# Optimization experiments

Hardware: AMD Instinct MI355X
Metric: run time of the kernel (lower is better)

The kernel has to match this reference:

```python
import jax, jax.numpy as jnp
import numpy as np

D_MODEL = 128; D_STATE = 64; D_CONV = 4; EXPAND = 2; HEADDIM = 32; NGROUPS = 1
D_INNER = EXPAND * D_MODEL            # 256
NHEADS = D_INNER // HEADDIM           # 8
CONV_DIM = D_INNER + 2 * NGROUPS * D_STATE   # 384 (x, B, C streams)
D_IN_PROJ = 2 * D_INNER + 2 * NGROUPS * D_STATE + NHEADS  # 648 (z, xBC, dt)
EPS = 1e-5


def setup_inputs() -> dict:
    key = jax.random.key(0)
    ks = jax.random.split(key, 8)
    B, L = 8, 4096
    x = jax.random.normal(ks[0], (B, L, D_MODEL), jnp.float32)
    norm_w = jnp.ones((D_MODEL,), jnp.float32)
    in_proj_w = jax.random.normal(ks[1], (D_IN_PROJ, D_MODEL), jnp.float32) * (D_MODEL ** -0.5)
    conv_w = jax.random.normal(ks[2], (CONV_DIM, D_CONV), jnp.float32) * (D_CONV ** -0.5)
    conv_b = jnp.zeros((CONV_DIM,), jnp.float32)
    dt_bias = jax.random.uniform(ks[3], (NHEADS,), jnp.float32, -4.0, -1.0)
    A_log = jnp.log(jax.random.uniform(ks[4], (NHEADS,), jnp.float32, 1.0, 16.0))
    D = jnp.ones((NHEADS,), jnp.float32)
    gnorm_w = jnp.ones((D_INNER,), jnp.float32)
    out_proj_w = jax.random.normal(ks[5], (D_MODEL, D_INNER), jnp.float32) * (D_INNER ** -0.5)
    return dict(x=x, norm_w=norm_w, in_proj_w=in_proj_w, conv_w=conv_w, conv_b=conv_b,
                dt_bias=dt_bias, A_log=A_log, D=D, gnorm_w=gnorm_w, out_proj_w=out_proj_w)


def _rmsnorm(x, w):
    return x * jax.lax.rsqrt(jnp.mean(x * x, axis=-1, keepdims=True) + EPS) * w


def _causal_dw_conv(x, w, b):
    # x: [B,L,C]; w: [C,K]; depthwise causal conv along L
    K = w.shape[1]
    xp = jnp.pad(x, ((0, 0), (K - 1, 0), (0, 0)))
    kern = jnp.transpose(w)[:, None, :]  # [K,1,C] for WIO with groups=C
    out = jax.lax.conv_general_dilated(
        xp, kern, window_strides=(1,), padding='VALID',
        dimension_numbers=('NWC', 'WIO', 'NWC'),
        feature_group_count=w.shape[0])
    return out + b


def _ssm(xh, dt, Bm, Cm, A):
    # xh: [B,L,H,P]; dt: [B,L,H]; Bm, Cm: [B,L,N]; A: [H]
    def step(h, inp):
        x_t, dt_t, B_t, C_t = inp
        dA = jnp.exp(dt_t * A)                                   # [B,H]
        h = h * dA[..., None, None] + (dt_t[..., None] * x_t)[..., None] * B_t[:, None, None, :]
        y = jnp.einsum('bhpn,bn->bhp', h, C_t)
        return h, y
    Bsz, L, H, P = xh.shape
    N = Bm.shape[-1]
    h0 = jnp.zeros((Bsz, H, P, N), xh.dtype)
    xs = (xh.transpose(1, 0, 2, 3), dt.transpose(1, 0, 2),
          Bm.transpose(1, 0, 2), Cm.transpose(1, 0, 2))
    _, ys = jax.lax.scan(step, h0, xs)
    return ys.transpose(1, 0, 2, 3)  # [B,L,H,P]


def reference(x, norm_w, in_proj_w, conv_w, conv_b, dt_bias, A_log, D, gnorm_w, out_proj_w):
    xn = _rmsnorm(x, norm_w)
    zxbcdt = xn @ in_proj_w.T                                    # [B,L,648]
    z, xBC, dt = jnp.split(zxbcdt, [D_INNER, D_INNER + CONV_DIM], axis=-1)
    dt = jax.nn.softplus(dt + dt_bias)                           # [B,L,H]
    xBC = jax.nn.silu(_causal_dw_conv(xBC, conv_w, conv_b))
    xs, Bm, Cm = jnp.split(xBC, [D_INNER, D_INNER + NGROUPS * D_STATE], axis=-1)
    Bsz, L, _ = x.shape
    xh = xs.reshape(Bsz, L, NHEADS, HEADDIM)
    A = -jnp.exp(A_log)                                          # [H]
    y = _ssm(xh, dt, Bm, Cm, A) + D[None, None, :, None] * xh    # D skip per head
    y = y.reshape(Bsz, L, D_INNER)
    y = _rmsnorm(y * jax.nn.silu(z), gnorm_w)                    # gated RMSNorm
    out = y @ out_proj_w.T
    return x + out
```

## Files before the change

### kernel.cpp

```cpp
#include <hip/hip_runtime.h>

#define DM    128
#define DI    256
#define NH    8
#define HD    32
#define NS    64
#define CDIM  384
#define DPROJ 648
#define LSEQ  4096
#define NB    8
#define NTOK  32768
#define LC    64
#define NC    64
#define EPSF  1e-5f
#define LOG2E 1.4426950408889634f

typedef __bf16 bf16;
typedef bf16  bf16x8 __attribute__((ext_vector_type(8)));
typedef bf16  bf16x4 __attribute__((ext_vector_type(4)));
typedef short short8 __attribute__((ext_vector_type(8)));
typedef float f32x4  __attribute__((ext_vector_type(4)));

__device__ __forceinline__ unsigned short f2bfbits(float f) {
    unsigned int u = __float_as_uint(f);
    unsigned int r = u + 0x7FFFu + ((u >> 16) & 1u);
    return (unsigned short)(r >> 16);
}
__device__ __forceinline__ float bfbits2f(unsigned short u) {
    return __uint_as_float(((unsigned int)u) << 16);
}

__global__ __launch_bounds__(256) void k_prep(const float* __restrict__ w1,
                                              const float* __restrict__ w2,
                                              const float* __restrict__ gw,
                                              unsigned short* __restrict__ w1g,
                                              unsigned short* __restrict__ w2f) {
    int i = blockIdx.x * 256 + threadIdx.x;
    if (i < 640 * DM) {
        int f = i >> 9, r = i & 511;
        int lane = r >> 3, jj = r & 7;
        int ns = f >> 2, kk = f & 3;
        int n = ns * 16 + (lane & 15), k = kk * 32 + (lane >> 4) * 8 + jj;
        w1g[i] = f2bfbits(w1[(size_t)n * DM + k]);
    } else {
        int j = i - 640 * DM;
        if (j < DM * DI) {
            int f = j >> 9, r = j & 511;
            int lane = r >> 3, jj = r & 7;
            int kk = f >> 3, nt = f & 7;
            int fr = lane & 15, ko = lane >> 4;
            int n = nt * 16 + fr, k = kk * 32 + ko * 8 + jj;
            w2f[j] = f2bfbits(w2[(size_t)n * DI + k] * gw[k]);
        }
    }
}

__global__ __launch_bounds__(256) void k_rmsdt(const float* __restrict__ x,
                                               const float* __restrict__ w,
                                               const float* __restrict__ w1,
                                               const float* __restrict__ dtb,
                                               unsigned short* __restrict__ xnb,
                                               float* __restrict__ dtf) {
    __shared__ float Xs[4][132];
    __shared__ float Wd[8][132];
    const int t = threadIdx.x;
    {
        int row = t >> 5, col = (t & 31) * 4;
        *(float4*)&Wd[row][col] = *(const float4*)(w1 + (size_t)(640 + row) * DM + col);
    }
    const int wave = t >> 6, lane = t & 63;
    const size_t row = (size_t)blockIdx.x * 4 + wave;
    const float* xr = x + row * DM + lane * 2;
    float v0 = xr[0], v1 = xr[1];
    float ss = v0 * v0 + v1 * v1;
    #pragma unroll
    for (int o = 32; o; o >>= 1) ss += __shfl_xor(ss, o);
    float r = rsqrtf(ss * (1.0f / DM) + EPSF);
    float o0 = v0 * r * w[lane * 2], o1 = v1 * r * w[lane * 2 + 1];
    Xs[wave][lane * 2] = o0; Xs[wave][lane * 2 + 1] = o1;
    ushort2 ob; ob.x = f2bfbits(o0); ob.y = f2bfbits(o1);
    *(ushort2*)(xnb + row * DM + lane * 2) = ob;
    __syncthreads();
    const int h = lane >> 3, ks = lane & 7;
    float acc = 0.f;
    #pragma unroll
    for (int i = 0; i < 4; i++) {
        float4 xv = *(const float4*)&Xs[wave][ks * 16 + i * 4];
        float4 wv = *(const float4*)&Wd[h][ks * 16 + i * 4];
        acc = fmaf(xv.x, wv.x, acc);
        acc = fmaf(xv.y, wv.y, acc);
        acc = fmaf(xv.z, wv.z, acc);
        acc = fmaf(xv.w, wv.w, acc);
    }
    acc += __shfl_xor(acc, 1);
    acc += __shfl_xor(acc, 2);
    acc += __shfl_xor(acc, 4);
    if (ks == 0) {
        float v = acc + dtb[h];
        dtf[row * NH + h] = (v > 20.f) ? v : log1pf(expf(v));
    }
}

__global__ __launch_bounds__(256, 4) void k_gemm1(const unsigned short* __restrict__ A,
                                                  const unsigned short* __restrict__ w1g,
                                                  unsigned short* __restrict__ zb,
                                                  unsigned short* __restrict__ xbc) {
    const int t = threadIdx.x;
    const int m0 = blockIdx.x * 64;
    const int wave = t >> 6, lane = t & 63;
    const int wm = wave >> 1, wn = wave & 1;
    const int fr = lane & 15, ko = lane >> 4;
    bf16x8 a[2][4];
    #pragma unroll
    for (int mt = 0; mt < 2; mt++)
        #pragma unroll
        for (int kk = 0; kk < 4; kk++)
            a[mt][kk] = *(const bf16x8*)(A + (size_t)(m0 + wm * 32 + mt * 16 + fr) * DM
                                           + kk * 32 + ko * 8);
    for (int nt = 0; nt < 10; nt++) {
        const unsigned short* wb = w1g + (((size_t)(nt * 4 + wn * 2) * 4) << 9) + lane * 8;
        f32x4 acc[2][2] = {};
        #pragma unroll
        for (int kk = 0; kk < 4; kk++) {
            bf16x8 b0 = *(const bf16x8*)(wb + ((size_t)kk << 9));
            bf16x8 b1 = *(const bf16x8*)(wb + ((size_t)(4 + kk) << 9));
            acc[0][0] = __builtin_amdgcn_mfma_f32_16x16x32_bf16(a[0][kk], b0, acc[0][0], 0, 0, 0);
            acc[1][0] = __builtin_amdgcn_mfma_f32_16x16x32_bf16(a[1][kk], b0, acc[1][0], 0, 0, 0);
            acc[0][1] = __builtin_amdgcn_mfma_f32_16x16x32_bf16(a[0][kk], b1, acc[0][1], 0, 0, 0);
            acc[1][1] = __builtin_amdgcn_mfma_f32_16x16x32_bf16(a[1][kk], b1, acc[1][1], 0, 0, 0);
        }
        unsigned short* dst; int ld, nc0;
        if (nt < 4) { dst = zb;  ld = DI;   nc0 = nt * 64; }
        else        { dst = xbc; ld = CDIM; nc0 = nt * 64 - 256; }
        #pragma unroll
        for (int mt = 0; mt < 2; mt++)
            #pragma unroll
            for (int ntt = 0; ntt < 2; ntt++) {
                int n = nc0 + wn * 32 + ntt * 16 + fr;
                #pragma unroll
                for (int rr = 0; rr < 4; rr++) {
                    int m = m0 + wm * 32 + mt * 16 + ko * 4 + rr;
                    dst[(size_t)m * ld + n] = f2bfbits(acc[mt][ntt][rr]);
                }
            }
    }
}

__global__ __launch_bounds__(384) void k_conv(const unsigned short* __restrict__ xbc,
                                              const float* __restrict__ cw,
                                              const float* __restrict__ cb,
                                              unsigned short* __restrict__ bcA,
                                              unsigned short* __restrict__ xT,
                                              unsigned short* __restrict__ bT) {
    __shared__ __align__(16) unsigned short L[320][72];
    const int c = threadIdx.x;
    const int t0 = blockIdx.x * 64;
    const int l0 = t0 & (LSEQ - 1);
    float4 wv = *(const float4*)(cw + c * 4);
    float bias = cb[c];
    const unsigned short* in = xbc + (size_t)t0 * CDIM + c;
    float h1 = 0.f, h2 = 0.f, h3 = 0.f;
    if (l0) {
        h1 = bfbits2f(in[-CDIM]);
        h2 = bfbits2f(in[-2 * CDIM]);
        h3 = bfbits2f(in[-3 * CDIM]);
    }
    short8 pk;
    #pragma unroll 8
    for (int t = 0; t < 64; t++) {
        float x0 = bfbits2f(in[(size_t)t * CDIM]);
        float acc = bias;
        acc = fmaf(x0, wv.w, acc);
        acc = fmaf(h1, wv.z, acc);
        acc = fmaf(h2, wv.y, acc);
        acc = fmaf(h3, wv.x, acc);
        float s = acc / (1.f + expf(-acc));
        unsigned short us = f2bfbits(s);
        if (c >= 256) bcA[(size_t)(t0 + t) * 128 + (c - 256)] = us;
        pk[t & 7] = (short)us;
        if (c < 320 && (t & 7) == 7) *(short8*)&L[c][t - 7] = pk;
        h3 = h2; h2 = h1; h1 = x0;
    }
    __syncthreads();
    #pragma unroll
    for (int it = 0; it < 7; it++) {
        int idx = it * 384 + c;
        if (idx < 2560) {
            int row = idx >> 3, tc = (idx & 7) * 8;
            short8 v = *(const short8*)&L[row][tc];
            unsigned short* dst = (row < 256)
                ? xT + (size_t)row * NTOK + t0 + tc
                : bT + (size_t)(row - 256) * NTOK + t0 + tc;
            *(short8*)dst = v;
        }
    }
}

__global__ __launch_bounds__(256, 4) void k_ssd1(const unsigned short* __restrict__ bT,
                                                 const unsigned short* __restrict__ xT,
                                                 const float* __restrict__ dtf,
                                                 const float* __restrict__ alog,
                                                 unsigned short* __restrict__ hst,
                                                 float* __restrict__ dAp) {
    __shared__ __align__(16) float wl[4][64];
    const int bh = blockIdx.x >> 4, cg = blockIdx.x & 15;
    const int b = bh >> 3, h = bh & 7;
    const int wave = threadIdx.x >> 6, lane = threadIdx.x & 63;
    const int c = cg * 4 + wave;
    const size_t tok0 = (size_t)b * LSEQ + c * LC;
    const float A = -expf(alog[h]);
    float dt = dtf[(tok0 + lane) * NH + h];
    float q = dt * A * LOG2E;
    #pragma unroll
    for (int o = 1; o <= 32; o <<= 1) {
        float tmp = __shfl_up(q, o);
        if (lane >= o) q += tmp;
    }
    float qL = __shfl(q, 63);
    wl[wave][lane] = exp2f(qL - q) * dt;
    if (lane == 0) dAp[(size_t)bh * NC + c] = exp2f(qL);
    __syncthreads();
    const int m = lane & 15, ko = lane >> 4;
    f32x4 hacc[4][2] = {};
    #pragma unroll
    for (int kh = 0; kh < 2; kh++) {
        bf16x8 xb[2];
        #pragma unroll
        for (int pi = 0; pi < 2; pi++)
            xb[pi] = *(const bf16x8*)(xT + (size_t)(h * HD + pi * 16 + m) * NTOK + tok0 + kh * 32 + ko * 8);
        f32x4 w0 = *(const f32x4*)&wl[wave][kh * 32 + ko * 8];
        f32x4 w1 = *(const f32x4*)&wl[wave][kh * 32 + ko * 8 + 4];
        #pragma unroll
        for (int ni = 0; ni < 4; ni++) {
            bf16x8 bv = *(const bf16x8*)(bT + (size_t)(ni * 16 + m) * NTOK + tok0 + kh * 32 + ko * 8);
            bf16x8 af;
            #pragma unroll
            for (int j = 0; j < 4; j++) af[j] = (bf16)((float)bv[j] * w0[j]);
            #pragma unroll
            for (int j = 0; j < 4; j++) af[4 + j] = (bf16)((float)bv[4 + j] * w1[j]);
            #pragma unroll
            for (int pi = 0; pi < 2; pi++)
                hacc[ni][pi] = __builtin_amdgcn_mfma_f32_16x16x32_bf16(af, xb[pi], hacc[ni][pi], 0, 0, 0);
        }
    }
    unsigned short* hb = hst + (((size_t)bh * NC + c) << 11);
    #pragma unroll
    for (int ni = 0; ni < 4; ni++)
        #pragma unroll
        for (int pi = 0; pi < 2; pi++) {
            bf16x4 pv;
            #pragma unroll
            for (int r = 0; r < 4; r++) pv[r] = (bf16)hacc[ni][pi][r];
            *(bf16x4*)(hb + (pi * 16 + m) * 64 + ni * 16 + ko * 4) = pv;
        }
}

__global__ __launch_bounds__(256) void k_ssm2(unsigned short* __restrict__ hst,
                                              const float* __restrict__ dAp) {
    __shared__ float dl[NC];
    const int bh = blockIdx.x >> 3, seg = blockIdx.x & 7;
    const int s = seg * 256 + threadIdx.x;
    if (threadIdx.x < NC) dl[threadIdx.x] = dAp[(size_t)bh * NC + threadIdx.x];
    __syncthreads();
    unsigned short* p = hst + ((size_t)bh * NC << 11) + s;
    float r = 0.f;
    float v0 = bfbits2f(p[0]);
    float v1 = bfbits2f(p[(size_t)1 << 11]);
    float v2 = bfbits2f(p[(size_t)2 << 11]);
    float v3 = bfbits2f(p[(size_t)3 << 11]);
    for (int c = 0; c < NC; c += 4) {
        float t;
        t = v0; if (c + 4 < NC) v0 = bfbits2f(p[(size_t)(c + 4) << 11]);
        p[(size_t)c << 11] = f2bfbits(r);       r = fmaf(r, dl[c], t);
        t = v1; if (c + 5 < NC) v1 = bfbits2f(p[(size_t)(c + 5) << 11]);
        p[(size_t)(c + 1) << 11] = f2bfbits(r); r = fmaf(r, dl[c + 1], t);
        t = v2; if (c + 6 < NC) v2 = bfbits2f(p[(size_t)(c + 6) << 11]);
        p[(size_t)(c + 2) << 11] = f2bfbits(r); r = fmaf(r, dl[c + 2], t);
        t = v3; if (c + 7 < NC) v3 = bfbits2f(p[(size_t)(c + 7) << 11]);
        p[(size_t)(c + 3) << 11] = f2bfbits(r); r = fmaf(r, dl[c + 3], t);
    }
}

__global__ __launch_bounds__(256, 2) void k_ssd3(const unsigned short* __restrict__ bcA,
                                                 const unsigned short* __restrict__ xT,
                                                 const float* __restrict__ dtf,
                                                 const float* __restrict__ alog,
                                                 const unsigned short* __restrict__ hst,
                                                 const float* __restrict__ Dw,
                                                 unsigned short* __restrict__ ybb) {
    __shared__ __align__(16) bf16 Pl[4][64 * 72];
    __shared__ __align__(16) float ql[4][64];
    __shared__ __align__(16) float dl[4][64];
    const int bh = blockIdx.x >> 4, cg = blockIdx.x & 15;
    const int b = bh >> 3, h = bh & 7;
    const int wave = threadIdx.x >> 6, lane = threadIdx.x & 63;
    const int c = cg * 4 + wave;
    const size_t tok0 = (size_t)b * LSEQ + c * LC;
    const float A = -expf(alog[h]);
    const float Dh = Dw[h];
    float dt = dtf[(tok0 + lane) * NH + h];
    float q = dt * A * LOG2E;
    #pragma unroll
    for (int o = 1; o <= 32; o <<= 1) {
        float tmp = __shfl_up(q, o);
        if (lane >= o) q += tmp;
    }
    ql[wave][lane] = q;
    dl[wave][lane] = dt;
    const int m = lane & 15, ko = lane >> 4;
    bf16x8 cf[4][2];
    #pragma unroll
    for (int ti = 0; ti < 4; ti++)
        #pragma unroll
        for (int kh = 0; kh < 2; kh++)
            cf[ti][kh] = *(const bf16x8*)(bcA + (tok0 + ti * 16 + m) * 128 + 64 + kh * 32 + ko * 8);
    f32x4 gt[4][4] = {};
    #pragma unroll
    for (int kh = 0; kh < 2; kh++) {
        bf16x8 bfg[4];
        #pragma unroll
        for (int si = 0; si < 4; si++)
            bfg[si] = *(const bf16x8*)(bcA + (tok0 + si * 16 + m) * 128 + kh * 32 + ko * 8);
        #pragma unroll
        for (int ti = 0; ti < 4; ti++)
            #pragma unroll
            for (int si = 0; si < 4; si++)
                gt[ti][si] = __builtin_amdgcn_mfma_f32_16x16x32_bf16(bfg[si], cf[ti][kh], gt[ti][si], 0, 0, 0);
    }
    __syncthreads();
    float qt[4];
    #pragma unroll
    for (int ti = 0; ti < 4; ti++) qt[ti] = ql[wave][ti * 16 + m];
    #pragma unroll
    for (int si = 0; si < 4; si++) {
        f32x4 qs = *(const f32x4*)&ql[wave][si * 16 + ko * 4];
        f32x4 ds = *(const f32x4*)&dl[wave][si * 16 + ko * 4];
        #pragma unroll
        for (int ti = 0; ti < 4; ti++) {
            bf16x4 pv = {};
            if (si <= ti) {
                const int t = ti * 16 + m;
                #pragma unroll
                for (int r = 0; r < 4; r++) {
                    int s = si * 16 + ko * 4 + r;
                    float p = 0.f;
                    if (s <= t) {
                        p = exp2f(qt[ti] - qs[r]) * ds[r] * gt[ti][si][r];
                        if (s == t) p += Dh;
                    }
                    pv[r] = (bf16)p;
                }
            }
            *(bf16x4*)&Pl[wave][(ti * 16 + m) * 72 + si * 16 + ko * 4] = pv;
        }
    }
    __syncthreads();
    f32x4 et[4];
    #pragma unroll
    for (int ti = 0; ti < 4; ti++) {
        f32x4 qv = *(const f32x4*)&ql[wave][ti * 16 + ko * 4];
        #pragma unroll
        for (int r = 0; r < 4; r++) et[ti][r] = exp2f(qv[r]);
    }
    const size_t hbase = ((size_t)bh * NC + c) << 11;
    f32x4 ya[4][2] = {}, ua[4][2] = {};
    #pragma unroll
    for (int kh = 0; kh < 2; kh++) {
        bf16x8 xb[2], hb2[2];
        #pragma unroll
        for (int pi = 0; pi < 2; pi++) {
            xb[pi]  = *(const bf16x8*)(xT + (size_t)(h * HD + pi * 16 + m) * NTOK + tok0 + kh * 32 + ko * 8);
            hb2[pi] = *(const bf16x8*)(hst + hbase + (pi * 16 + m) * 64 + kh * 32 + ko * 8);
        }
        #pragma unroll
        for (int ti = 0; ti < 4; ti++) {
            bf16x8 pa = *(const bf16x8*)&Pl[wave][(ti * 16 + m) * 72 + kh * 32 + ko * 8];
            #pragma unroll
            for (int pi = 0; pi < 2; pi++) {
                ya[ti][pi] = __builtin_amdgcn_mfma_f32_16x16x32_bf16(pa, xb[pi], ya[ti][pi], 0, 0, 0);
                ua[ti][pi] = __builtin_amdgcn_mfma_f32_16x16x32_bf16(cf[ti][kh], hb2[pi], ua[ti][pi], 0, 0, 0);
            }
        }
    }
    unsigned short* yrow = ybb + tok0 * DI + h * HD;
    #pragma unroll
    for (int ti = 0; ti < 4; ti++)
        #pragma unroll
        for (int pi = 0; pi < 2; pi++)
            #pragma unroll
            for (int r = 0; r < 4; r++) {
                int t = ti * 16 + ko * 4 + r;
                yrow[(size_t)t * DI + pi * 16 + m] =
                    f2bfbits(ya[ti][pi][r] + et[ti][r] * ua[ti][pi][r]);
            }
}

__global__ __launch_bounds__(256, 4) void k_gemm2g(const unsigned short* __restrict__ ybb,
                                                   const unsigned short* __restrict__ zb,
                                                   const unsigned short* __restrict__ w2f,
                                                   const float* __restrict__ xin,
                                                   float* __restrict__ out) {
    const int t = threadIdx.x;
    const int wave = t >> 6, lane = t & 63;
    const int fr = lane & 15, ko = lane >> 4;
    const int m0 = blockIdx.x * 64 + wave * 16;
    const size_t rowo = (size_t)(m0 + fr) * DI;
    float ss = 0.f;
    bf16x8 gb[8];
    #pragma unroll
    for (int kk = 0; kk < 8; kk++) {
        int co = kk * 32 + ko * 8;
        bf16x8 yv = *(const bf16x8*)(ybb + rowo + co);
        bf16x8 zv = *(const bf16x8*)(zb + rowo + co);
        #pragma unroll
        for (int j = 0; j < 8; j++) {
            float z = (float)zv[j];
            float g = (float)yv[j] * (z / (1.f + expf(-z)));
            ss += g * g;
            gb[kk][j] = (bf16)g;
        }
    }
    ss += __shfl_xor(ss, 16);
    ss += __shfl_xor(ss, 32);
    const float rs = rsqrtf(ss * (1.0f / DI) + EPSF);
    #pragma unroll
    for (int kk = 0; kk < 8; kk++)
        #pragma unroll
        for (int j = 0; j < 8; j++)
            gb[kk][j] = (bf16)((float)gb[kk][j] * rs);
    const unsigned short* wp = w2f + (size_t)lane * 8;
    f32x4 acc[8] = {};
    #pragma unroll
    for (int kk = 0; kk < 8; kk++) {
        #pragma unroll
        for (int nt = 0; nt < 8; nt++) {
            bf16x8 bfr = *(const bf16x8*)(wp + (((size_t)kk * 8 + nt) << 9));
            acc[nt] = __builtin_amdgcn_mfma_f32_16x16x32_bf16(gb[kk], bfr, acc[nt], 0, 0, 0);
        }
    }
    #pragma unroll
    for (int nt = 0; nt < 8; nt++) {
        int n = nt * 16 + fr;
        #pragma unroll
        for (int rr = 0; rr < 4; rr++) {
            int m = m0 + ko * 4 + rr;
            out[(size_t)m * DM + n] = xin[(size_t)m * DM + n] + acc[nt][rr];
        }
    }
}

extern "C" void kernel_launch(void* const* d_in, const int* in_sizes, int n_in,
                              void* d_out, int out_size, void* d_ws, size_t ws_size,
                              hipStream_t stream) {
    const float* x   = (const float*)d_in[0];
    const float* nw  = (const float*)d_in[1];
    const float* w1  = (const float*)d_in[2];
    const float* cw  = (const float*)d_in[3];
    const float* cb  = (const float*)d_in[4];
    const float* dtb = (const float*)d_in[5];
    const float* al  = (const float*)d_in[6];
    const float* Dw  = (const float*)d_in[7];
    const float* gw  = (const float*)d_in[8];
    const float* w2  = (const float*)d_in[9];
    float* out = (float*)d_out;

    float* ws = (float*)d_ws;
    float*  dAp = ws;
    float*  dtf = dAp + NB * NH * NC;
    unsigned short* hst = (unsigned short*)(dtf + (size_t)NTOK * NH);
    unsigned short* zb  = hst + (size_t)NB * NH * NC * 2048;
    unsigned short* xbc = zb + (size_t)NTOK * DI;
    unsigned short* bcA = xbc + (size_t)NTOK * CDIM;
    unsigned short* xT  = bcA + (size_t)NTOK * 128;
    unsigned short* bT  = xT + (size_t)DI * NTOK;
    unsigned short* ybb = bT + (size_t)64 * NTOK;
    unsigned short* w1g = ybb + (size_t)NTOK * DI;
    unsigned short* w2f = w1g + (size_t)640 * DM;
    unsigned short* xnb = ybb;

    k_prep<<<(640 * DM + DM * DI + 255) / 256, 256, 0, stream>>>(w1, w2, gw, w1g, w2f);
    k_rmsdt<<<NTOK / 4, 256, 0, stream>>>(x, nw, w1, dtb, xnb, dtf);
    k_gemm1<<<NTOK / 64, 256, 0, stream>>>(xnb, w1g, zb, xbc);
    k_conv<<<NTOK / 64, 384, 0, stream>>>(xbc, cw, cb, bcA, xT, bT);
    k_ssd1<<<NB * NH * (NC / 4), 256, 0, stream>>>(bT, xT, dtf, al, hst, dAp);
    k_ssm2<<<NB * NH * 8, 256, 0, stream>>>(hst, dAp);
    k_ssd3<<<NB * NH * (NC / 4), 256, 0, stream>>>(bcA, xT, dtf, al, hst, Dw, ybb);
    k_gemm2g<<<NTOK / 64, 256, 0, stream>>>(ybb, zb, w2f, x, out);
}
```

Before: 197.1 us.

## Fuse RMSNorm and dt projection into GEMM1 and drop intra-wave barriers

```diff
diff --git a/kernel.cpp b/kernel.cpp
--- a/kernel.cpp
+++ b/kernel.cpp
@@ -55,68 +55,74 @@
     }
 }
 
-__global__ __launch_bounds__(256) void k_rmsdt(const float* __restrict__ x,
-                                               const float* __restrict__ w,
-                                               const float* __restrict__ w1,
-                                               const float* __restrict__ dtb,
-                                               unsigned short* __restrict__ xnb,
-                                               float* __restrict__ dtf) {
-    __shared__ float Xs[4][132];
+__global__ __launch_bounds__(256, 4) void k_gemm1(const float* __restrict__ x,
+                                                  const float* __restrict__ nw,
+                                                  const float* __restrict__ w1,
+                                                  const float* __restrict__ dtb,
+                                                  const unsigned short* __restrict__ w1g,
+                                                  unsigned short* __restrict__ zb,
+                                                  unsigned short* __restrict__ xbc,
+                                                  float* __restrict__ dtf) {
+    __shared__ float Xs[64][132];
     __shared__ float Wd[8][132];
     const int t = threadIdx.x;
+    const int wave = t >> 6, lane = t & 63;
+    const int m0 = blockIdx.x * 64;
     {
         int row = t >> 5, col = (t & 31) * 4;
         *(float4*)&Wd[row][col] = *(const float4*)(w1 + (size_t)(640 + row) * DM + col);
     }
-    const int wave = t >> 6, lane = t & 63;
-    const size_t row = (size_t)blockIdx.x * 4 + wave;
-    const float* xr = x + row * DM + lane * 2;
-    float v0 = xr[0], v1 = xr[1];
-    float ss = v0 * v0 + v1 * v1;
-    #pragma unroll
-    for (int o = 32; o; o >>= 1) ss += __shfl_xor(ss, o);
-    float r = rsqrtf(ss * (1.0f / DM) + EPSF);
-    float o0 = v0 * r * w[lane * 2], o1 = v1 * r * w[lane * 2 + 1];
-    Xs[wave][lane * 2] = o0; Xs[wave][lane * 2 + 1] = o1;
-    ushort2 ob; ob.x = f2bfbits(o0); ob.y = f2bfbits(o1);
-    *(ushort2*)(xnb + row * DM + lane * 2) = ob;
+    const float nw0 = nw[lane * 2], nw1 = nw[lane * 2 + 1];
+    #pragma unroll
+    for (int i = 0; i < 16; i++) {
+        int r = wave * 16 + i;
+        const float* xr = x + (size_t)(m0 + r) * DM + lane * 2;
+        float v0 = xr[0], v1 = xr[1];
+        float ss = v0 * v0 + v1 * v1;
+        #pragma unroll
+        for (int o = 32; o; o >>= 1) ss += __shfl_xor(ss, o);
+        float rs = rsqrtf(ss * (1.0f / DM) + EPSF);
+        Xs[r][lane * 2]     = v0 * rs * nw0;
+        Xs[r][lane * 2 + 1] = v1 * rs * nw1;
+    }
     __syncthreads();
-    const int h = lane >> 3, ks = lane & 7;
-    float acc = 0.f;
-    #pragma unroll
-    for (int i = 0; i < 4; i++) {
-        float4 xv = *(const float4*)&Xs[wave][ks * 16 + i * 4];
-        float4 wv = *(const float4*)&Wd[h][ks * 16 + i * 4];
-        acc = fmaf(xv.x, wv.x, acc);
-        acc = fmaf(xv.y, wv.y, acc);
-        acc = fmaf(xv.z, wv.z, acc);
-        acc = fmaf(xv.w, wv.w, acc);
-    }
-    acc += __shfl_xor(acc, 1);
-    acc += __shfl_xor(acc, 2);
-    acc += __shfl_xor(acc, 4);
-    if (ks == 0) {
-        float v = acc + dtb[h];
-        dtf[row * NH + h] = (v > 20.f) ? v : log1pf(expf(v));
-    }
-}
-
-__global__ __launch_bounds__(256, 4) void k_gemm1(const unsigned short* __restrict__ A,
-                                                  const unsigned short* __restrict__ w1g,
-                                                  unsigned short* __restrict__ zb,
-                                                  unsigned short* __restrict__ xbc) {
-    const int t = threadIdx.x;
-    const int m0 = blockIdx.x * 64;
-    const int wave = t >> 6, lane = t & 63;
+    {
+        const int h = lane >> 3, ks = lane & 7;
+        const float dtbh = dtb[h];
+        #pragma unroll
+        for (int i = 0; i < 16; i++) {
+            int r = wave * 16 + i;
+            float acc = 0.f;
+            #pragma unroll
+            for (int q = 0; q < 4; q++) {
+                float4 xv = *(const float4*)&Xs[r][ks * 16 + q * 4];
+                float4 wv = *(const float4*)&Wd[h][ks * 16 + q * 4];
+                acc = fmaf(xv.x, wv.x, acc); acc = fmaf(xv.y, wv.y, acc);
+                acc = fmaf(xv.z, wv.z, acc); acc = fmaf(xv.w, wv.w, acc);
+            }
+            acc += __shfl_xor(acc, 1);
+            acc += __shfl_xor(acc, 2);
+            acc += __shfl_xor(acc, 4);
+            if (ks == 0) {
+                float v = acc + dtbh;
+                dtf[(size_t)(m0 + r) * NH + h] = (v > 20.f) ? v : log1pf(expf(v));
+            }
+        }
+    }
     const int wm = wave >> 1, wn = wave & 1;
     const int fr = lane & 15, ko = lane >> 4;
     bf16x8 a[2][4];
     #pragma unroll
     for (int mt = 0; mt < 2; mt++)
         #pragma unroll
-        for (int kk = 0; kk < 4; kk++)
-            a[mt][kk] = *(const bf16x8*)(A + (size_t)(m0 + wm * 32 + mt * 16 + fr) * DM
-                                           + kk * 32 + ko * 8);
+        for (int kk = 0; kk < 4; kk++) {
+            const float* src = &Xs[wm * 32 + mt * 16 + fr][kk * 32 + ko * 8];
+            float4 lo = *(const float4*)src, hi = *(const float4*)(src + 4);
+            bf16x8 af;
+            af[0] = (bf16)lo.x; af[1] = (bf16)lo.y; af[2] = (bf16)lo.z; af[3] = (bf16)lo.w;
+            af[4] = (bf16)hi.x; af[5] = (bf16)hi.y; af[6] = (bf16)hi.z; af[7] = (bf16)hi.w;
+            a[mt][kk] = af;
+        }
     for (int nt = 0; nt < 10; nt++) {
         const unsigned short* wb = w1g + (((size_t)(nt * 4 + wn * 2) * 4) << 9) + lane * 8;
         f32x4 acc[2][2] = {};
@@ -219,7 +225,6 @@
     float qL = __shfl(q, 63);
     wl[wave][lane] = exp2f(qL - q) * dt;
     if (lane == 0) dAp[(size_t)bh * NC + c] = exp2f(qL);
-    __syncthreads();
     const int m = lane & 15, ko = lane >> 4;
     f32x4 hacc[4][2] = {};
     #pragma unroll
@@ -327,7 +332,6 @@
             for (int si = 0; si < 4; si++)
                 gt[ti][si] = __builtin_amdgcn_mfma_f32_16x16x32_bf16(bfg[si], cf[ti][kh], gt[ti][si], 0, 0, 0);
     }
-    __syncthreads();
     float qt[4];
     #pragma unroll
     for (int ti = 0; ti < 4; ti++) qt[ti] = ql[wave][ti * 16 + m];
@@ -354,7 +358,6 @@
             *(bf16x4*)&Pl[wave][(ti * 16 + m) * 72 + si * 16 + ko * 4] = pv;
         }
     }
-    __syncthreads();
     f32x4 et[4];
     #pragma unroll
     for (int ti = 0; ti < 4; ti++) {
@@ -476,11 +479,9 @@
     unsigned short* ybb = bT + (size_t)64 * NTOK;
     unsigned short* w1g = ybb + (size_t)NTOK * DI;
     unsigned short* w2f = w1g + (size_t)640 * DM;
-    unsigned short* xnb = ybb;
 
     k_prep<<<(640 * DM + DM * DI + 255) / 256, 256, 0, stream>>>(w1, w2, gw, w1g, w2f);
-    k_rmsdt<<<NTOK / 4, 256, 0, stream>>>(x, nw, w1, dtb, xnb, dtf);
-    k_gemm1<<<NTOK / 64, 256, 0, stream>>>(xnb, w1g, zb, xbc);
+    k_gemm1<<<NTOK / 64, 256, 0, stream>>>(x, nw, w1, dtb, w1g, zb, xbc, dtf);
     k_conv<<<NTOK / 64, 384, 0, stream>>>(xbc, cw, cb, bcA, xT, bT);
     k_ssd1<<<NB * NH * (NC / 4), 256, 0, stream>>>(bT, xT, dtf, al, hst, dAp);
     k_ssm2<<<NB * NH * 8, 256, 0, stream>>>(hst, dAp);
```

New measurement: 194.2 us. Within noise of the previous version (-1.4%).
